# Kernel tuning notes

Measured on AMD Instinct MI355X. Metric: run time of the kernel, lower is better.

The kernel has to match this reference:

```python
import jax, jax.numpy as jnp
import numpy as np

B, T, C, H = 2, 2048, 1024, 16
HS = C // H  # head size = 64


def _rope_cos_sin(t, hs):
    # theta_i = 1/10000^(2(i-1)/hs) for i in [1, hs/2]
    pos = jnp.arange(t, dtype=jnp.float32)[:, None]          # [T,1]
    i = jnp.arange(1, hs // 2 + 1, dtype=jnp.float32)[None]  # [1,hs/2]
    theta = 1.0 / 10000.0 ** (2.0 * (i - 1.0) / hs)
    ang = pos * theta                                        # [T,hs/2]
    return jnp.cos(ang), jnp.sin(ang)


def _apply_rope(u, cos, sin):
    # u: [B,H,T,HS]; complex multiply on consecutive pairs
    u2 = u.reshape(*u.shape[:-1], HS // 2, 2)
    x0, x1 = u2[..., 0], u2[..., 1]
    c = cos[None, None]  # [1,1,T,hs/2]
    s = sin[None, None]
    r0 = x0 * c - x1 * s
    r1 = x0 * s + x1 * c
    return jnp.stack([r0, r1], axis=-1).reshape(u.shape)


def setup_inputs() -> dict:
    key = jax.random.key(0)
    ks = jax.random.split(key, 5)
    return {
        "x": jax.random.normal(ks[0], (B, T, C), dtype=jnp.float32),
        "W_qkv": jax.random.normal(ks[1], (C, 3 * C), dtype=jnp.float32) * 0.02,
        "b_qkv": jax.random.normal(ks[2], (3 * C,), dtype=jnp.float32) * 0.02,
        "W_proj": jax.random.normal(ks[3], (C, C), dtype=jnp.float32) * 0.02,
        "b_proj": jax.random.normal(ks[4], (C,), dtype=jnp.float32) * 0.02,
    }


def reference(x, W_qkv, b_qkv, W_proj, b_proj):
    b, t, c = x.shape
    qkv = x @ W_qkv + b_qkv                                   # [B,T,3C]
    qkv = qkv.reshape(b, t, H, 3 * HS).transpose(0, 2, 1, 3)  # [B,H,T,3*HS]
    q, k, v = jnp.split(qkv, 3, axis=-1)                      # each [B,H,T,HS]

    cos, sin = _rope_cos_sin(t, HS)
    q = _apply_rope(q, cos, sin)
    k = _apply_rope(k, cos, sin)

    att = jnp.einsum("bhqd,bhkd->bhqk", q, k) / jnp.sqrt(jnp.float32(HS))
    causal = jnp.tril(jnp.ones((t, t), dtype=bool))[None, None]
    att = jnp.where(causal, att, jnp.float32(-1e9))
    att = jax.nn.softmax(att, axis=-1)
    y = jnp.einsum("bhqk,bhkd->bhqd", att, v)                 # [B,H,T,HS]
    y = y.transpose(0, 2, 1, 3).reshape(b, t, c)
    return y @ W_proj + b_proj
```

## Files before the change

kernel.cpp:

```cpp
#include <hip/hip_runtime.h>

typedef unsigned short u16;
typedef unsigned int u32;
typedef __bf16 bf16x8 __attribute__((ext_vector_type(8)));
typedef float f32x4 __attribute__((ext_vector_type(4)));
typedef u16 u16x4 __attribute__((ext_vector_type(4)));
typedef u16 u16x8 __attribute__((ext_vector_type(8)));

__device__ __forceinline__ u16 f2bf(float f) {
  u32 u = __builtin_bit_cast(u32, f);
  u += 0x7fffu + ((u >> 16) & 1u);
  return (u16)(u >> 16);
}

__device__ __forceinline__ u32 pk2(float a, float b) {
  u32 ua = __builtin_bit_cast(u32, a) + 0x8000u;
  u32 ub = __builtin_bit_cast(u32, b) + 0x8000u;
  return __builtin_amdgcn_perm(ub, ua, 0x07060302);
}

__device__ __forceinline__ void gld16(const void* g, void* l) {
  __builtin_amdgcn_global_load_lds(
      (const __attribute__((address_space(1))) void*)g,
      (__attribute__((address_space(3))) void*)l, 16, 0, 0);
}

__global__ __launch_bounds__(256) void k_prep(
    const float* __restrict__ x, u16* __restrict__ xb,
    const float* __restrict__ Wqkv, u16* __restrict__ Wqkvt,
    const float* __restrict__ Wproj, u16* __restrict__ Wpt,
    float2* __restrict__ rope) {
  __shared__ float tile[32][33];
  const int tid = threadIdx.x;
  int bx = blockIdx.x;
  if (bx < 4096) {
    int i = (bx * 256 + tid) * 4;
    float4 v = *(const float4*)(x + i);
    u16x4 o = { f2bf(v.x), f2bf(v.y), f2bf(v.z), f2bf(v.w) };
    *(u16x4*)(xb + i) = o;
    return;
  }
  bx -= 4096;
  const float* src; u16* dst; int R, Cc, bxx, byy;
  if (bx < 3072) {
    src = Wqkv; dst = Wqkvt; R = 1024; Cc = 3072; bxx = bx % 96; byy = bx / 96;
  } else if (bx < 4096) {
    int b = bx - 3072;
    src = Wproj; dst = Wpt; R = 1024; Cc = 1024; bxx = b % 32; byy = b / 32;
  } else {
    int i = (bx - 4096) * 256 + tid;
    int t = i >> 5, d = i & 31;
    float theta = expf(-(float)d * 0.28782313662425575f);
    float ang = (float)t * theta;
    rope[i] = make_float2(cosf(ang), sinf(ang));
    return;
  }
  int xx = tid & 31, yy = tid >> 5;
  int c0 = bxx * 32, r0 = byy * 32;
  for (int i = 0; i < 4; ++i)
    tile[yy + 8 * i][xx] = src[(size_t)(r0 + yy + 8 * i) * Cc + c0 + xx];
  __syncthreads();
  for (int i = 0; i < 4; ++i)
    dst[(size_t)(c0 + yy + 8 * i) * R + r0 + xx] = f2bf(tile[xx][yy + 8 * i]);
}

__global__ __launch_bounds__(256, 4) void k_qkv(
    const u16* __restrict__ Xb,
    const u16* __restrict__ Wt,
    const float* __restrict__ bias,
    const float2* __restrict__ rope,
    u16* __restrict__ Qg,
    u16* __restrict__ Kg,
    u16* __restrict__ Vt) {
  __shared__ alignas(16) u16 smem[18432];
  u16* As = smem;
  u16* Bs = smem + 8192;
  const int tid = threadIdx.x;
  const int lane = tid & 63, w = tid >> 6;
  const int quad = lane >> 4, l15 = lane & 15;
  const int m0 = blockIdx.y * 128, n0 = blockIdx.x * 128;
  const int wm = (w & 1) * 64, wn = (w >> 1) * 64;
  const int srow = lane >> 3, sj = lane & 7;
  const int sw = (sj ^ srow) * 8;
  const f32x4 vzero = {0.f, 0.f, 0.f, 0.f};

  f32x4 acc[4][4];
  for (int i = 0; i < 4; ++i)
    for (int j = 0; j < 4; ++j) acc[i][j] = vzero;

  for (int kt = 0; kt < 1024; kt += 64) {
    __syncthreads();
    for (int i = 0; i < 4; ++i) {
      int row = w * 32 + i * 8;
      gld16(Xb + (size_t)(m0 + row + srow) * 1024 + kt + sw, &As[row * 64]);
      gld16(Wt + (size_t)(n0 + row + srow) * 1024 + kt + sw, &Bs[row * 64]);
    }
    __syncthreads();
    for (int ks = 0; ks < 2; ++ks) {
      const int cc = ((ks * 4 + quad) ^ (l15 & 7)) * 8;
      bf16x8 a[4], b[4];
      for (int mt = 0; mt < 4; ++mt)
        a[mt] = *(const bf16x8*)&As[(wm + mt * 16 + l15) * 64 + cc];
      for (int nt = 0; nt < 4; ++nt)
        b[nt] = *(const bf16x8*)&Bs[(wn + nt * 16 + l15) * 64 + cc];
      for (int nt = 0; nt < 4; ++nt)
        for (int mt = 0; mt < 4; ++mt)
          acc[nt][mt] = __builtin_amdgcn_mfma_f32_16x16x32_bf16(
              b[nt], a[mt], acc[nt][mt], 0, 0, 0);
    }
  }
  __syncthreads();

  const int half = w >> 1;
  const int nh = n0 + half * 64;
  const int region = (nh % 192) >> 6;
  u16* Eh = smem + half * 9216;
  if (region < 2) {
    for (int nt = 0; nt < 4; ++nt) {
      float4 bv4 = *(const float4*)&bias[nh + nt * 16 + quad * 4];
      for (int mt = 0; mt < 4; ++mt) {
        int m_l = wm + mt * 16 + l15;
        int t = (m0 + m_l) & 2047;
        float4 cs = *(const float4*)&rope[t * 32 + nt * 8 + quad * 2];
        float v0 = acc[nt][mt][0] + bv4.x;
        float v1 = acc[nt][mt][1] + bv4.y;
        float v2 = acc[nt][mt][2] + bv4.z;
        float v3 = acc[nt][mt][3] + bv4.w;
        float r0 = fmaf(-v1, cs.y, v0 * cs.x);
        float r1 = fmaf( v0, cs.y, v1 * cs.x);
        float r2 = fmaf(-v3, cs.w, v2 * cs.z);
        float r3 = fmaf( v2, cs.w, v3 * cs.z);
        uint2 pv; pv.x = pk2(r0, r1); pv.y = pk2(r2, r3);
        *(uint2*)&Eh[m_l * 72 + nt * 16 + quad * 4] = pv;
      }
    }
  } else {
    for (int nt = 0; nt < 4; ++nt) {
      float4 bv4 = *(const float4*)&bias[nh + nt * 16 + quad * 4];
      for (int mt = 0; mt < 4; ++mt) {
        int m_l = wm + mt * 16 + l15;
        int cb = nt * 16 + quad * 4;
        Eh[(cb + 0) * 136 + m_l] = f2bf(acc[nt][mt][0] + bv4.x);
        Eh[(cb + 1) * 136 + m_l] = f2bf(acc[nt][mt][1] + bv4.y);
        Eh[(cb + 2) * 136 + m_l] = f2bf(acc[nt][mt][2] + bv4.z);
        Eh[(cb + 3) * 136 + m_l] = f2bf(acc[nt][mt][3] + bv4.w);
      }
    }
  }
  __syncthreads();

  const int bb = m0 >> 11, t0 = m0 & 2047;
  for (int hf = 0; hf < 2; ++hf) {
    const int nhf = n0 + hf * 64;
    const int hh = nhf / 192;
    const int reg = (nhf % 192) >> 6;
    const u16* Ef = smem + hf * 9216;
    if (reg < 2) {
      u16* dst = (reg == 0 ? Qg : Kg) +
                 ((size_t)(bb * 16 + hh) * 2048 + t0) * 64;
      int chunk = tid & 7, row0 = tid >> 3;
      for (int p = 0; p < 4; ++p) {
        int row = row0 + p * 32;
        u16x8 val = *(const u16x8*)&Ef[row * 72 + chunk * 8];
        *(u16x8*)(dst + (size_t)row * 64 + chunk * 8) = val;
      }
    } else {
      u16* dstv = Vt + (size_t)(bb * 16 + hh) * 64 * 2048 + t0;
      int mch = tid & 15, c0r = tid >> 4;
      for (int p = 0; p < 4; ++p) {
        int c = c0r + p * 16;
        u16x8 val = *(const u16x8*)&Ef[c * 136 + mch * 8];
        *(u16x8*)(dstv + (size_t)c * 2048 + mch * 8) = val;
      }
    }
  }
}

__global__ __launch_bounds__(256, 4) void k_attn(
    const u16* __restrict__ Qg, const u16* __restrict__ Kg,
    const u16* __restrict__ Vt, u16* __restrict__ Og) {
  __shared__ alignas(16) u16 Ks[2][64 * 64];
  __shared__ alignas(16) u16 Vs[2][64 * 64];
  __shared__ alignas(16) u16 Ps[64 * 72];
  const int tid = threadIdx.x, lane = tid & 63, w = tid >> 6;
  const int quad = lane >> 4, l15 = lane & 15;
  const int id = blockIdx.x;
  const int xr = id & 7, j = id >> 3;
  const int bx = j & 15;
  const int bh = (j >> 4) * 8 + xr;
  const u16* Qh = Qg + (size_t)bh * 2048 * 64;
  const u16* Kh = Kg + (size_t)bh * 2048 * 64;
  const u16* Vh = Vt + (size_t)bh * 64 * 2048;
  const f32x4 vzero = {0.f, 0.f, 0.f, 0.f};
  const float SCL = 0.125f * 1.4426950408889634f;
  const int myrow = w * 16;
  const int bb = bh >> 4, h = bh & 15;

  const int r8 = lane >> 3, j8 = lane & 7;
  const int sw_c = (j8 ^ r8) * 8;

  for (int i = 0; i < 2; ++i) {
    int row = w * 16 + i * 8;
    gld16(Kh + (size_t)(row + r8) * 64 + sw_c, &Ks[0][row * 64]);
    gld16(Vh + (size_t)(row + r8) * 2048 + sw_c, &Vs[0][row * 64]);
  }

  int buf = 0;
  const int tiles[2] = {bx, 31 - bx};
  for (int ti = 0; ti < 2; ++ti) {
    const int qt = tiles[ti];
    const int q0 = qt * 64;
    bf16x8 aq[2];
    {
      const u16* qp = Qh + (size_t)(q0 + myrow + l15) * 64 + quad * 8;
      aq[0] = *(const bf16x8*)(qp);
      aq[1] = *(const bf16x8*)(qp + 32);
    }
    float lsum = 0.f;
    f32x4 O[4];
    for (int nt = 0; nt < 4; ++nt) O[nt] = vzero;

    const int nk = qt + 1;
    for (int kb = 0; kb < nk; ++kb) {
      const int k0 = kb * 64;
      __syncthreads();
      int nxt = (kb + 1 < nk) ? (k0 + 64) : (ti == 0 ? 0 : -1);
      if (nxt >= 0) {
        for (int i = 0; i < 2; ++i) {
          int row = w * 16 + i * 8;
          gld16(Kh + (size_t)(nxt + row + r8) * 64 + sw_c, &Ks[buf ^ 1][row * 64]);
          gld16(Vh + (size_t)(row + r8) * 2048 + nxt + sw_c, &Vs[buf ^ 1][row * 64]);
        }
      }

      f32x4 st[4];
      for (int nt = 0; nt < 4; ++nt) st[nt] = vzero;
      for (int ks = 0; ks < 2; ++ks) {
        bf16x8 ak[4];
        for (int nt = 0; nt < 4; ++nt)
          ak[nt] = *(const bf16x8*)&Ks[buf][(nt * 16 + l15) * 64 +
                                           ((ks * 4 + quad) ^ (l15 & 7)) * 8];
        for (int nt = 0; nt < 4; ++nt)
          st[nt] = __builtin_amdgcn_mfma_f32_16x16x32_bf16(ak[nt], aq[ks], st[nt], 0, 0, 0);
      }

      if (kb < qt) {
        for (int nt = 0; nt < 4; ++nt) {
          float p0 = __builtin_amdgcn_exp2f(st[nt][0] * SCL);
          float p1 = __builtin_amdgcn_exp2f(st[nt][1] * SCL);
          float p2 = __builtin_amdgcn_exp2f(st[nt][2] * SCL);
          float p3 = __builtin_amdgcn_exp2f(st[nt][3] * SCL);
          lsum += (p0 + p1) + (p2 + p3);
          uint2 pv; pv.x = pk2(p0, p1); pv.y = pk2(p2, p3);
          *(uint2*)&Ps[(myrow + l15) * 72 + nt * 16 + quad * 4] = pv;
        }
      } else {
        const int tq = q0 + myrow + l15;
        const int kbase = k0 + quad * 4;
        for (int nt = 0; nt < 4; ++nt) {
          float p[4];
          for (int r = 0; r < 4; ++r) {
            float pv = __builtin_amdgcn_exp2f(st[nt][r] * SCL);
            p[r] = (kbase + nt * 16 + r <= tq) ? pv : 0.f;
            lsum += p[r];
          }
          uint2 pv; pv.x = pk2(p[0], p[1]); pv.y = pk2(p[2], p[3]);
          *(uint2*)&Ps[(myrow + l15) * 72 + nt * 16 + quad * 4] = pv;
        }
      }

      for (int ks = 0; ks < 2; ++ks) {
        bf16x8 a = *(const bf16x8*)&Ps[(myrow + l15) * 72 + ks * 32 + quad * 8];
        bf16x8 bv[4];
        for (int nt = 0; nt < 4; ++nt)
          bv[nt] = *(const bf16x8*)&Vs[buf][(nt * 16 + l15) * 64 +
                                           ((ks * 4 + quad) ^ (l15 & 7)) * 8];
        for (int nt = 0; nt < 4; ++nt)
          O[nt] = __builtin_amdgcn_mfma_f32_16x16x32_bf16(a, bv[nt], O[nt], 0, 0, 0);
      }
      buf ^= 1;
    }

    float ls = lsum;
    ls += __shfl_xor(ls, 16, 64);
    ls += __shfl_xor(ls, 32, 64);
    float inv[4];
    for (int r = 0; r < 4; ++r)
      inv[r] = 1.0f / __shfl(ls, quad * 4 + r, 16);

    for (int nt = 0; nt < 4; ++nt)
      for (int r = 0; r < 4; ++r)
        Ps[(myrow + quad * 4 + r) * 72 + nt * 16 + l15] = f2bf(O[nt][r] * inv[r]);
    __syncthreads();
    u16* dst = Og + ((size_t)bb * 2048 + q0) * 1024 + h * 64;
    int chunk = tid & 7, row0 = tid >> 3;
    for (int p = 0; p < 2; ++p) {
      int row = row0 + p * 32;
      u16x8 val = *(const u16x8*)&Ps[row * 72 + chunk * 8];
      *(u16x8*)(dst + (size_t)row * 1024 + chunk * 8) = val;
    }
  }
}

__global__ __launch_bounds__(256, 4) void k_proj(
    const u16* __restrict__ Ag,
    const u16* __restrict__ Wt,
    const float* __restrict__ bias,
    float* __restrict__ out) {
  __shared__ alignas(16) u16 As[64 * 64];
  __shared__ alignas(16) u16 Bs[128 * 64];
  const int tid = threadIdx.x;
  const int lane = tid & 63, w = tid >> 6;
  const int quad = lane >> 4, l15 = lane & 15;
  const int m0 = blockIdx.y * 64, n0 = blockIdx.x * 128;
  const int wm = (w & 1) * 32, wn = (w >> 1) * 64;
  const int srow = lane >> 3, sj = lane & 7;
  const int sw = (sj ^ srow) * 8;
  const f32x4 vzero = {0.f, 0.f, 0.f, 0.f};

  f32x4 acc[2][4];
  for (int i = 0; i < 2; ++i)
    for (int j = 0; j < 4; ++j) acc[i][j] = vzero;

  for (int kt = 0; kt < 1024; kt += 64) {
    __syncthreads();
    for (int i = 0; i < 2; ++i) {
      int row = w * 16 + i * 8;
      gld16(Ag + (size_t)(m0 + row + srow) * 1024 + kt + sw, &As[row * 64]);
    }
    for (int i = 0; i < 4; ++i) {
      int row = w * 32 + i * 8;
      gld16(Wt + (size_t)(n0 + row + srow) * 1024 + kt + sw, &Bs[row * 64]);
    }
    __syncthreads();
    for (int ks = 0; ks < 2; ++ks) {
      const int cc = ((ks * 4 + quad) ^ (l15 & 7)) * 8;
      bf16x8 a[2], b[4];
      for (int mt = 0; mt < 2; ++mt)
        a[mt] = *(const bf16x8*)&As[(wm + mt * 16 + l15) * 64 + cc];
      for (int nt = 0; nt < 4; ++nt)
        b[nt] = *(const bf16x8*)&Bs[(wn + nt * 16 + l15) * 64 + cc];
      for (int mt = 0; mt < 2; ++mt)
        for (int nt = 0; nt < 4; ++nt)
          acc[mt][nt] = __builtin_amdgcn_mfma_f32_16x16x32_bf16(
              a[mt], b[nt], acc[mt][nt], 0, 0, 0);
    }
  }

  for (int nt = 0; nt < 4; ++nt) {
    int n = n0 + wn + nt * 16 + l15;
    float bv = bias[n];
    for (int mt = 0; mt < 2; ++mt)
      for (int r = 0; r < 4; ++r) {
        int m = m0 + wm + mt * 16 + quad * 4 + r;
        out[(size_t)m * 1024 + n] = acc[mt][nt][r] + bv;
      }
  }
}

extern "C" void kernel_launch(void* const* d_in, const int* in_sizes, int n_in,
                              void* d_out, int out_size, void* d_ws, size_t ws_size,
                              hipStream_t stream) {
  (void)in_sizes; (void)n_in; (void)out_size; (void)ws_size;
  const float* x     = (const float*)d_in[0];
  const float* Wqkv  = (const float*)d_in[1];
  const float* bqkv  = (const float*)d_in[2];
  const float* Wproj = (const float*)d_in[3];
  const float* bproj = (const float*)d_in[4];
  float* out = (float*)d_out;

  char* ws = (char*)d_ws;
  size_t off = 0;
  u16* Xb    = (u16*)(ws + off); off += (size_t)4096 * 1024 * 2;
  u16* Wqkvt = (u16*)(ws + off); off += (size_t)3072 * 1024 * 2;
  u16* Wpt   = (u16*)(ws + off); off += (size_t)1024 * 1024 * 2;
  u16* Qg    = (u16*)(ws + off); off += (size_t)2 * 16 * 2048 * 64 * 2;
  u16* Kg    = (u16*)(ws + off); off += (size_t)2 * 16 * 2048 * 64 * 2;
  u16* Vt    = (u16*)(ws + off); off += (size_t)2 * 16 * 64 * 2048 * 2;
  u16* Att   = (u16*)(ws + off); off += (size_t)4096 * 1024 * 2;
  float2* rope = (float2*)(ws + off); off += (size_t)2048 * 32 * sizeof(float2);

  k_prep<<<8448, 256, 0, stream>>>(x, Xb, Wqkv, Wqkvt, Wproj, Wpt, rope);
  k_qkv<<<dim3(24, 32), 256, 0, stream>>>(Xb, Wqkvt, bqkv, rope, Qg, Kg, Vt);
  k_attn<<<512, 256, 0, stream>>>(Qg, Kg, Vt, Att);
  k_proj<<<dim3(8, 64), 256, 0, stream>>>(Att, Wpt, bproj, out);
}
```

Baseline: 167.8 us.

## Split attention into one query tile per block with XOR-swizzled P buffer

The attention kernel now launches 1024 blocks that each handle a single query tile, instead of 512 blocks that each process a paired tile (bx, 31-bx). A bit-mixing block-id mapping interleaves long and short causal tiles across blocks to spread the work. The padded P/O staging buffer (stride 72) is replaced by a 64-stride buffer with an XOR swizzle, which shrinks LDS use and should avoid bank conflicts. The trade-off is less balanced per-block work, and the K/V prefetch across tile pairs is lost, while the extra blocks may raise occupancy and improve load distribution.

New measurement: 173.5 us. 1.03x slower.

```diff
diff --git a/kernel.cpp b/kernel.cpp
--- a/kernel.cpp
+++ b/kernel.cpp
@@ -181,13 +181,16 @@
     const u16* __restrict__ Vt, u16* __restrict__ Og) {
   __shared__ alignas(16) u16 Ks[2][64 * 64];
   __shared__ alignas(16) u16 Vs[2][64 * 64];
-  __shared__ alignas(16) u16 Ps[64 * 72];
+  __shared__ alignas(16) u16 Ps[64 * 64];
   const int tid = threadIdx.x, lane = tid & 63, w = tid >> 6;
   const int quad = lane >> 4, l15 = lane & 15;
   const int id = blockIdx.x;
   const int xr = id & 7, j = id >> 3;
-  const int bx = j & 15;
-  const int bh = (j >> 4) * 8 + xr;
+  const int b0 = j & 1, b5 = (j >> 5) & 1;
+  const int x5 = ((j >> 1) & 15) | (((j >> 6) & 1) << 4);
+  const int qt = (b0 ^ b5) ? x5 : (31 - x5);
+  const int bh = xr + 8 * ((b0 << 1) | b5);
+  const int q0 = qt * 64;
   const u16* Qh = Qg + (size_t)bh * 2048 * 64;
   const u16* Kh = Kg + (size_t)bh * 2048 * 64;
   const u16* Vh = Vt + (size_t)bh * 64 * 2048;
@@ -195,9 +198,22 @@
   const float SCL = 0.125f * 1.4426950408889634f;
   const int myrow = w * 16;
   const int bb = bh >> 4, h = bh & 15;
+  const int ph = (l15 & 7) << 3;
 
   const int r8 = lane >> 3, j8 = lane & 7;
   const int sw_c = (j8 ^ r8) * 8;
+  const int cc0 = (quad ^ (l15 & 7)) * 8;
+  const int cc1 = ((4 + quad) ^ (l15 & 7)) * 8;
+
+  bf16x8 aq[2];
+  {
+    const u16* qp = Qh + (size_t)(q0 + myrow + l15) * 64 + quad * 8;
+    aq[0] = *(const bf16x8*)(qp);
+    aq[1] = *(const bf16x8*)(qp + 32);
+  }
+  float lsum = 0.f;
+  f32x4 O[4];
+  for (int nt = 0; nt < 4; ++nt) O[nt] = vzero;
 
   for (int i = 0; i < 2; ++i) {
     int row = w * 16 + i * 8;
@@ -206,99 +222,95 @@
   }
 
   int buf = 0;
-  const int tiles[2] = {bx, 31 - bx};
-  for (int ti = 0; ti < 2; ++ti) {
-    const int qt = tiles[ti];
-    const int q0 = qt * 64;
-    bf16x8 aq[2];
+  const int nk = qt + 1;
+  for (int kb = 0; kb < nk; ++kb) {
+    const int k0 = kb * 64;
+    __syncthreads();
+    if (kb + 1 < nk) {
+      const int nxt = k0 + 64;
+      for (int i = 0; i < 2; ++i) {
+        int row = w * 16 + i * 8;
+        gld16(Kh + (size_t)(nxt + row + r8) * 64 + sw_c, &Ks[buf ^ 1][row * 64]);
+        gld16(Vh + (size_t)(row + r8) * 2048 + nxt + sw_c, &Vs[buf ^ 1][row * 64]);
+      }
+    }
+
+    f32x4 st[4];
+    for (int nt = 0; nt < 4; ++nt) st[nt] = vzero;
     {
-      const u16* qp = Qh + (size_t)(q0 + myrow + l15) * 64 + quad * 8;
-      aq[0] = *(const bf16x8*)(qp);
-      aq[1] = *(const bf16x8*)(qp + 32);
-    }
-    float lsum = 0.f;
-    f32x4 O[4];
-    for (int nt = 0; nt < 4; ++nt) O[nt] = vzero;
-
-    const int nk = qt + 1;
-    for (int kb = 0; kb < nk; ++kb) {
-      const int k0 = kb * 64;
-      __syncthreads();
-      int nxt = (kb + 1 < nk) ? (k0 + 64) : (ti == 0 ? 0 : -1);
-      if (nxt >= 0) {
-        for (int i = 0; i < 2; ++i) {
-          int row = w * 16 + i * 8;
-          gld16(Kh + (size_t)(nxt + row + r8) * 64 + sw_c, &Ks[buf ^ 1][row * 64]);
-          gld16(Vh + (size_t)(row + r8) * 2048 + nxt + sw_c, &Vs[buf ^ 1][row * 64]);
+      bf16x8 ak[4];
+      for (int nt = 0; nt < 4; ++nt)
+        ak[nt] = *(const bf16x8*)&Ks[buf][(nt * 16 + l15) * 64 + cc0];
+      for (int nt = 0; nt < 4; ++nt)
+        st[nt] = __builtin_amdgcn_mfma_f32_16x16x32_bf16(ak[nt], aq[0], st[nt], 0, 0, 0);
+      for (int nt = 0; nt < 4; ++nt)
+        ak[nt] = *(const bf16x8*)&Ks[buf][(nt * 16 + l15) * 64 + cc1];
+      for (int nt = 0; nt < 4; ++nt)
+        st[nt] = __builtin_amdgcn_mfma_f32_16x16x32_bf16(ak[nt], aq[1], st[nt], 0, 0, 0);
+    }
+
+    if (kb < qt) {
+      for (int nt = 0; nt < 4; ++nt) {
+        float p0 = __builtin_amdgcn_exp2f(st[nt][0] * SCL);
+        float p1 = __builtin_amdgcn_exp2f(st[nt][1] * SCL);
+        float p2 = __builtin_amdgcn_exp2f(st[nt][2] * SCL);
+        float p3 = __builtin_amdgcn_exp2f(st[nt][3] * SCL);
+        lsum += (p0 + p1) + (p2 + p3);
+        uint2 pv; pv.x = pk2(p0, p1); pv.y = pk2(p2, p3);
+        *(uint2*)&Ps[(myrow + l15) * 64 + ((nt * 16 + quad * 4) ^ ph)] = pv;
+      }
+    } else {
+      const int tq = q0 + myrow + l15;
+      const int kbase = k0 + quad * 4;
+      for (int nt = 0; nt < 4; ++nt) {
+        float p[4];
+        for (int r = 0; r < 4; ++r) {
+          float pv = __builtin_amdgcn_exp2f(st[nt][r] * SCL);
+          p[r] = (kbase + nt * 16 + r <= tq) ? pv : 0.f;
+          lsum += p[r];
         }
-      }
-
-      f32x4 st[4];
-      for (int nt = 0; nt < 4; ++nt) st[nt] = vzero;
-      for (int ks = 0; ks < 2; ++ks) {
-        bf16x8 ak[4];
-        for (int nt = 0; nt < 4; ++nt)
-          ak[nt] = *(const bf16x8*)&Ks[buf][(nt * 16 + l15) * 64 +
-                                           ((ks * 4 + quad) ^ (l15 & 7)) * 8];
-        for (int nt = 0; nt < 4; ++nt)
-          st[nt] = __builtin_amdgcn_mfma_f32_16x16x32_bf16(ak[nt], aq[ks], st[nt], 0, 0, 0);
-      }
-
-      if (kb < qt) {
-        for (int nt = 0; nt < 4; ++nt) {
-          float p0 = __builtin_amdgcn_exp2f(st[nt][0] * SCL);
-          float p1 = __builtin_amdgcn_exp2f(st[nt][1] * SCL);
-          float p2 = __builtin_amdgcn_exp2f(st[nt][2] * SCL);
-          float p3 = __builtin_amdgcn_exp2f(st[nt][3] * SCL);
-          lsum += (p0 + p1) + (p2 + p3);
-          uint2 pv; pv.x = pk2(p0, p1); pv.y = pk2(p2, p3);
-          *(uint2*)&Ps[(myrow + l15) * 72 + nt * 16 + quad * 4] = pv;
-        }
-      } else {
-        const int tq = q0 + myrow + l15;
-        const int kbase = k0 + quad * 4;
-        for (int nt = 0; nt < 4; ++nt) {
-          float p[4];
-          for (int r = 0; r < 4; ++r) {
-            float pv = __builtin_amdgcn_exp2f(st[nt][r] * SCL);
-            p[r] = (kbase + nt * 16 + r <= tq) ? pv : 0.f;
-            lsum += p[r];
-          }
-          uint2 pv; pv.x = pk2(p[0], p[1]); pv.y = pk2(p[2], p[3]);
-          *(uint2*)&Ps[(myrow + l15) * 72 + nt * 16 + quad * 4] = pv;
-        }
-      }
-
-      for (int ks = 0; ks < 2; ++ks) {
-        bf16x8 a = *(const bf16x8*)&Ps[(myrow + l15) * 72 + ks * 32 + quad * 8];
-        bf16x8 bv[4];
-        for (int nt = 0; nt < 4; ++nt)
-          bv[nt] = *(const bf16x8*)&Vs[buf][(nt * 16 + l15) * 64 +
-                                           ((ks * 4 + quad) ^ (l15 & 7)) * 8];
-        for (int nt = 0; nt < 4; ++nt)
-          O[nt] = __builtin_amdgcn_mfma_f32_16x16x32_bf16(a, bv[nt], O[nt], 0, 0, 0);
-      }
-      buf ^= 1;
-    }
-
-    float ls = lsum;
-    ls += __shfl_xor(ls, 16, 64);
-    ls += __shfl_xor(ls, 32, 64);
-    float inv[4];
-    for (int r = 0; r < 4; ++r)
-      inv[r] = 1.0f / __shfl(ls, quad * 4 + r, 16);
-
-    for (int nt = 0; nt < 4; ++nt)
-      for (int r = 0; r < 4; ++r)
-        Ps[(myrow + quad * 4 + r) * 72 + nt * 16 + l15] = f2bf(O[nt][r] * inv[r]);
-    __syncthreads();
-    u16* dst = Og + ((size_t)bb * 2048 + q0) * 1024 + h * 64;
-    int chunk = tid & 7, row0 = tid >> 3;
-    for (int p = 0; p < 2; ++p) {
-      int row = row0 + p * 32;
-      u16x8 val = *(const u16x8*)&Ps[row * 72 + chunk * 8];
-      *(u16x8*)(dst + (size_t)row * 1024 + chunk * 8) = val;
-    }
+        uint2 pv; pv.x = pk2(p[0], p[1]); pv.y = pk2(p[2], p[3]);
+        *(uint2*)&Ps[(myrow + l15) * 64 + ((nt * 16 + quad * 4) ^ ph)] = pv;
+      }
+    }
+
+    {
+      bf16x8 a = *(const bf16x8*)&Ps[(myrow + l15) * 64 + ((quad * 8) ^ ph)];
+      bf16x8 bv[4];
+      for (int nt = 0; nt < 4; ++nt)
+        bv[nt] = *(const bf16x8*)&Vs[buf][(nt * 16 + l15) * 64 + cc0];
+      for (int nt = 0; nt < 4; ++nt)
+        O[nt] = __builtin_amdgcn_mfma_f32_16x16x32_bf16(a, bv[nt], O[nt], 0, 0, 0);
+      a = *(const bf16x8*)&Ps[(myrow + l15) * 64 + ((32 + quad * 8) ^ ph)];
+      for (int nt = 0; nt < 4; ++nt)
+        bv[nt] = *(const bf16x8*)&Vs[buf][(nt * 16 + l15) * 64 + cc1];
+      for (int nt = 0; nt < 4; ++nt)
+        O[nt] = __builtin_amdgcn_mfma_f32_16x16x32_bf16(a, bv[nt], O[nt], 0, 0, 0);
+    }
+    buf ^= 1;
+  }
+
+  lsum += __shfl_xor(lsum, 16, 64);
+  lsum += __shfl_xor(lsum, 32, 64);
+  float inv[4];
+  for (int r = 0; r < 4; ++r)
+    inv[r] = 1.0f / __shfl(lsum, quad * 4 + r, 16);
+
+  __syncthreads();
+  for (int nt = 0; nt < 4; ++nt)
+    for (int r = 0; r < 4; ++r) {
+      int row = myrow + quad * 4 + r;
+      int col = (nt * 16 + l15) ^ (((quad * 4 + r) & 7) << 3);
+      Ps[row * 64 + col] = f2bf(O[nt][r] * inv[r]);
+    }
+  __syncthreads();
+  u16* dst = Og + ((size_t)bb * 2048 + q0) * 1024 + h * 64;
+  int chunk = tid & 7, row0 = tid >> 3;
+  for (int p = 0; p < 2; ++p) {
+    int row = row0 + p * 32;
+    int col = (chunk * 8) ^ ((row & 7) << 3);
+    u16x8 val = *(const u16x8*)&Ps[row * 64 + col];
+    *(u16x8*)(dst + (size_t)row * 1024 + chunk * 8) = val;
   }
 }
 
@@ -382,6 +394,6 @@
 
   k_prep<<<8448, 256, 0, stream>>>(x, Xb, Wqkv, Wqkvt, Wproj, Wpt, rope);
   k_qkv<<<dim3(24, 32), 256, 0, stream>>>(Xb, Wqkvt, bqkv, rope, Qg, Kg, Vt);
-  k_attn<<<512, 256, 0, stream>>>(Qg, Kg, Vt, Att);
+  k_attn<<<1024, 256, 0, stream>>>(Qg, Kg, Vt, Att);
   k_proj<<<dim3(8, 64), 256, 0, stream>>>(Att, Wpt, bproj, out);
 }
```
